# Kernel optimization log

Measured on AMD Instinct MI355X. Metric: run time of the kernel, lower is better.

The kernel has to match this reference:

```python
import jax, jax.numpy as jnp
import numpy as np

D_MODEL = 768
D_LATENT = 12288
K = 20
N = 16384


def setup_inputs() -> dict:
    key = jax.random.key(0)
    k1, k2, k3, k4, k5 = jax.random.split(key, 5)
    x = jax.random.normal(k1, (N, D_MODEL), dtype=jnp.float32)
    # nn.Linear default init scale ~ 1/sqrt(fan_in)
    W_enc = jax.random.normal(k2, (D_LATENT, D_MODEL), dtype=jnp.float32) / np.sqrt(D_MODEL)
    b_enc = jax.random.normal(k3, (D_LATENT,), dtype=jnp.float32) * 0.01
    W_dec = jax.random.normal(k4, (D_MODEL, D_LATENT), dtype=jnp.float32) / np.sqrt(D_LATENT)
    b_dec = jax.random.normal(k5, (D_MODEL,), dtype=jnp.float32) * 0.01
    return {"x": x, "W_enc": W_enc, "b_enc": b_enc, "W_dec": W_dec, "b_dec": b_dec}


def reference(x, W_enc, b_enc, W_dec, b_dec):
    # encode: [N, 12288]
    latents = jnp.einsum('nd,ld->nl', x, W_enc) + b_enc
    # top-k(20) per row; scatter kept values back into zeros == latents * mask
    vals, idx = jax.lax.top_k(latents, K)            # [N, K]
    rows = jnp.arange(latents.shape[0])[:, None]      # [N, 1]
    sparse = jnp.zeros_like(latents).at[rows, idx].set(vals)
    # decode: [N, 768]
    recons = jnp.einsum('nl,dl->nd', sparse, W_dec) + b_dec
    return recons
```

## Files before the change

### kernel.cpp

```cpp
#include <hip/hip_runtime.h>
#include <hip/hip_bf16.h>
#include <stdint.h>

#define D_MODEL_  768
#define D_LATENT_ 12288
#define N_ROWS_   16384
#define TOPK_     20
#define TOPC      16
#define NQ        8
#define NC        128
#define AUTO      12
#define NREFW     16
#define THR0      1.7f

#define BM 256
#define BN 128
#define BK 64
#define KT (D_MODEL_ / BK)
#define CTQ (D_LATENT_ / NQ / BN)
#define NTHREADS 1024
#define CAP 8

#define BUFSZ 49152

typedef float f4 __attribute__((ext_vector_type(4)));
typedef short bf16x8 __attribute__((ext_vector_type(8)));

typedef const void __attribute__((address_space(1)))* gptr_t;
typedef void __attribute__((address_space(3)))* lptr_t;

__device__ __forceinline__ void stage16(const void* g, void* l) {
  __builtin_amdgcn_global_load_lds((gptr_t)g, (lptr_t)l, 16, 0, 0);
}

__device__ __forceinline__ unsigned short bf16_rne(float f) {
  unsigned u = __builtin_bit_cast(unsigned, f);
  u += 0x7FFFu + ((u >> 16) & 1u);
  return (unsigned short)(u >> 16);
}
__device__ __forceinline__ float bf16_to_f(unsigned short h) {
  return __builtin_bit_cast(float, ((unsigned)h) << 16);
}
__device__ __forceinline__ unsigned packcand(float v, int idx) {
  return v > 0.f ? (((unsigned)bf16_rne(v) << 16) | (unsigned)idx) : 0u;
}

#define BAR_LGKM() do { asm volatile("s_waitcnt lgkmcnt(0)" ::: "memory"); \
                        __builtin_amdgcn_s_barrier(); } while (0)

__global__ void tobf16_kernel(const float4* __restrict__ in, ushort4* __restrict__ o, int n4) {
  int i = blockIdx.x * blockDim.x + threadIdx.x;
  if (i >= n4) return;
  float4 v = in[i];
  ushort4 h;
  h.x = bf16_rne(v.x); h.y = bf16_rne(v.y); h.z = bf16_rne(v.z); h.w = bf16_rne(v.w);
  o[i] = h;
}

__global__ void transpose_bf16_kernel(const float* __restrict__ wd, unsigned short* __restrict__ wdT) {
  __shared__ float tile[32][33];
  const int l0 = blockIdx.x * 32;
  const int d0 = blockIdx.y * 32;
  const int tx = threadIdx.x, ty = threadIdx.y;
#pragma unroll
  for (int i = 0; i < 32; i += 8)
    tile[ty + i][tx] = wd[(size_t)(d0 + ty + i) * D_LATENT_ + l0 + tx];
  __syncthreads();
#pragma unroll
  for (int i = 0; i < 32; i += 8)
    wdT[(size_t)(l0 + ty + i) * D_MODEL_ + d0 + tx] = bf16_rne(tile[tx][ty + i]);
}

__global__ __launch_bounds__(NTHREADS, 4) void sae_topk(
    const unsigned short* __restrict__ xh, const unsigned short* __restrict__ wh,
    const float* __restrict__ b_enc, unsigned* __restrict__ candp)
{
  __shared__ __align__(16) unsigned char smem[2 * BUFSZ];
  __shared__ unsigned s_top[BM][TOPC];
  __shared__ unsigned s_cand[BM][CAP];
  __shared__ float    s_thr[BM];
  __shared__ int      s_cnt[BM];
  __shared__ int      s_flag;

  const int tid  = threadIdx.x;
  const int lane = tid & 63;
  const int wid  = tid >> 6;
  const int wm   = wid >> 2;
  const int wn   = wid & 3;
  const int quar = blockIdx.x & 7;
  const int brow = (blockIdx.x >> 3) * BM;
  const int cbase = quar * (D_LATENT_ / NQ);

  auto stage_tile = [&](int buf, int ct, int kt) {
    unsigned char* base = smem + buf * BUFSZ;
#pragma unroll
    for (int j = 0; j < 2; ++j) {
      const int cid = tid + j * 1024;
      const int row = cid >> 3, slot = cid & 7;
      stage16(xh + (size_t)(brow + row) * D_MODEL_ + kt * BK + (slot ^ (row & 7)) * 8,
              base + cid * 16);
    }
    {
      const int row = tid >> 3, slot = tid & 7;
      stage16(wh + (size_t)(cbase + ct * BN + row) * D_MODEL_ + kt * BK + (slot ^ (row & 7)) * 8,
              base + 32768 + tid * 16);
    }
  };

  stage_tile(0, 0, 0);

  if (tid < BM) { s_thr[tid] = THR0; s_cnt[tid] = 0; }
  if (tid == 0) s_flag = 0;
  for (int i = tid; i < BM * TOPC; i += NTHREADS) (&s_top[0][0])[i] = 0u;

  f4 acc[4][2];
#pragma unroll
  for (int m = 0; m < 4; ++m)
#pragma unroll
    for (int n = 0; n < 2; ++n) { f4 z = {0.f, 0.f, 0.f, 0.f}; acc[m][n] = z; }

  int cur = 0;
#pragma unroll 1
  for (int ct = 0; ct < CTQ; ++ct) {
    const float be0 = b_enc[cbase + ct * BN + wn * 32 + (lane & 15)];
    const float be1 = b_enc[cbase + ct * BN + wn * 32 + 16 + (lane & 15)];

#pragma unroll 1
    for (int kt = 0; kt < KT; ++kt) {
      bool more = true;
      if (kt < KT - 1)       stage_tile(cur ^ 1, ct, kt + 1);
      else if (ct + 1 < CTQ) stage_tile(cur ^ 1, ct + 1, 0);
      else                   more = false;
      if (more) { asm volatile("s_waitcnt vmcnt(3)" ::: "memory"); }
      else      { asm volatile("s_waitcnt vmcnt(0)" ::: "memory"); }
      __builtin_amdgcn_s_barrier();
      {
        const unsigned char* base = smem + cur * BUFSZ;
#pragma unroll
        for (int ks = 0; ks < 2; ++ks) {
          const int c = ks * 4 + (lane >> 4);
          bf16x8 ah[4], bh[2];
#pragma unroll
          for (int m = 0; m < 4; ++m) {
            const int row = wm * 64 + m * 16 + (lane & 15);
            ah[m] = *(const bf16x8*)(base + row * 128 + ((c ^ (row & 7)) << 4));
          }
#pragma unroll
          for (int n = 0; n < 2; ++n) {
            const int col = wn * 32 + n * 16 + (lane & 15);
            bh[n] = *(const bf16x8*)(base + 32768 + col * 128 + ((c ^ (col & 7)) << 4));
          }
#pragma unroll
          for (int m = 0; m < 4; ++m)
#pragma unroll
            for (int n = 0; n < 2; ++n)
              acc[m][n] = __builtin_amdgcn_mfma_f32_16x16x32_bf16(ah[m], bh[n], acc[m][n], 0, 0, 0);
        }
      }
      __builtin_amdgcn_s_barrier();
      cur ^= 1;
    }

#pragma unroll
    for (int m = 0; m < 4; ++m) {
      acc[m][0][0] += be0; acc[m][0][1] += be0; acc[m][0][2] += be0; acc[m][0][3] += be0;
      acc[m][1][0] += be1; acc[m][1][1] += be1; acc[m][1][2] += be1; acc[m][1][3] += be1;
    }

    unsigned pend = ~0u;
#pragma unroll 1
    for (;;) {
#pragma unroll
      for (int m = 0; m < 4; ++m)
#pragma unroll
        for (int n = 0; n < 2; ++n)
#pragma unroll
          for (int j = 0; j < 4; ++j) {
            const int b = m * 8 + n * 4 + j;
            if (pend & (1u << b)) {
              const int row = wm * 64 + m * 16 + ((lane >> 4) << 2) + j;
              const float v = acc[m][n][j];
              if (v <= s_thr[row]) {
                pend &= ~(1u << b);
              } else {
                const int pos = atomicAdd(&s_cnt[row], 1);
                if (pos < CAP) {
                  s_cand[row][pos] = packcand(v, cbase + ct * BN + wn * 32 + n * 16 + (lane & 15));
                  pend &= ~(1u << b);
                }
              }
            }
          }
      BAR_LGKM();
      if (tid < BM) {
        const int row = tid;
        const int nc = s_cnt[row];
        if (nc > 0) {
          if (nc > CAP) s_flag = 1;
          unsigned minp = s_top[row][0]; int mpos = 0;
#pragma unroll
          for (int k = 1; k < TOPC; ++k) { const unsigned t = s_top[row][k]; if (t < minp) { minp = t; mpos = k; } }
          const int ne = nc < CAP ? nc : CAP;
          for (int j = 0; j < ne; ++j) {
            const unsigned p = s_cand[row][j];
            if (p > minp) {
              s_top[row][mpos] = p;
              minp = s_top[row][0]; mpos = 0;
#pragma unroll
              for (int k = 1; k < TOPC; ++k) { const unsigned t = s_top[row][k]; if (t < minp) { minp = t; mpos = k; } }
            }
          }
          const float mv = bf16_to_f((unsigned short)(minp >> 16));
          s_thr[row] = mv > THR0 ? mv : THR0;
          s_cnt[row] = 0;
        }
      }
      BAR_LGKM();
      const int f = s_flag;
      BAR_LGKM();
      if (!f) break;
      if (tid == 0) s_flag = 0;
    }

#pragma unroll
    for (int m = 0; m < 4; ++m)
#pragma unroll
      for (int n = 0; n < 2; ++n) { f4 z = {0.f, 0.f, 0.f, 0.f}; acc[m][n] = z; }
  }

  if (tid < BM) {
#pragma unroll
    for (int k = 0; k < TOPC; ++k)
      candp[(size_t)(brow + tid) * NC + quar * TOPC + k] = s_top[tid][k];
  }
}

__device__ __forceinline__ float chunk_fma(const float* __restrict__ xr,
                                           const float* __restrict__ wr,
                                           int beg, int end) {
  float a = 0.f;
#pragma unroll 4
  for (int d0 = beg; d0 < end; d0 += 4) {
    const float4 xv = *(const float4*)(xr + d0);
    const float4 wv = *(const float4*)(wr + d0);
    a = fmaf(xv.x, wv.x, a);
    a = fmaf(xv.y, wv.y, a);
    a = fmaf(xv.z, wv.z, a);
    a = fmaf(xv.w, wv.w, a);
  }
  return a;
}

__global__ __launch_bounds__(256) void refine_decode13(
    const float* __restrict__ x, const float* __restrict__ W_enc,
    const float* __restrict__ b_enc, const unsigned* __restrict__ candp,
    const unsigned short* __restrict__ wdTb, const float* __restrict__ b_dec,
    float* __restrict__ out)
{
  __shared__ unsigned s_p[4][NC];
  __shared__ unsigned s_ref[4][NREFW];
  __shared__ float s_rv[4][NREFW];
  __shared__ int   s_rid[4][NREFW];
  __shared__ float s_selv[4][TOPK_];
  __shared__ int   s_seli[4][TOPK_];

  const int tid  = threadIdx.x;
  const int w    = tid >> 6;
  const int lane = tid & 63;
  const int row  = blockIdx.x * 4 + w;

  s_p[w][lane]      = candp[(size_t)row * NC + lane];
  s_p[w][lane + 64] = candp[(size_t)row * NC + lane + 64];
  if (lane < NREFW) s_ref[w][lane] = 0u;
  __syncthreads();

#pragma unroll
  for (int t = 0; t < 2; ++t) {
    const int i = lane + t * 64;
    const unsigned p = s_p[w][i];
    if (p != 0u) {
      int r = 0;
#pragma unroll 1
      for (int j = 0; j < NC; ++j) r += (s_p[w][j] > p);
      if (r < AUTO) {
        s_selv[w][r] = bf16_to_f((unsigned short)(p >> 16));
        s_seli[w][r] = (int)(p & 0x3FFFu);
      } else if (r < AUTO + NREFW) {
        s_ref[w][r - AUTO] = p;
      }
    }
  }
  __syncthreads();

  {
    const int cand  = lane & 15;
    const int chunk = lane >> 4;
    float part = 0.f;
    const unsigned p = s_ref[w][cand];
    if (p != 0u && chunk < 3) {
      const int idx = (int)(p & 0x3FFFu);
      const float* xr = x + (size_t)row * D_MODEL_;
      const float* wr = W_enc + (size_t)idx * D_MODEL_;
      const int beg = chunk == 0 ? 0 : (chunk == 1 ? 320 : 544);
      const int end = chunk == 0 ? 320 : (chunk == 1 ? 544 : 768);
      part = chunk_fma(xr, wr, beg, end);
    }
    const float a2 = __shfl(part, cand + 16);
    const float a3 = __shfl(part, cand + 32);
    if (chunk == 0 && lane < NREFW) {
      if (p != 0u) {
        s_rv[w][lane]  = ((part + a2) + a3) + b_enc[(int)(p & 0x3FFFu)];
        s_rid[w][lane] = (int)(p & 0x3FFFu);
      } else {
        s_rv[w][lane]  = -__builtin_inff();
        s_rid[w][lane] = -1;
      }
    }
  }
  __syncthreads();

  if (lane < NREFW) {
    const float v = s_rv[w][lane]; const int id = s_rid[w][lane];
    if (id >= 0) {
      int rank = 0;
#pragma unroll 1
      for (int j = 0; j < NREFW; ++j) {
        const float vj = s_rv[w][j];
        rank += (vj > v) || (vj == v && s_rid[w][j] > id);
      }
      if (rank < TOPK_ - AUTO) { s_selv[w][AUTO + rank] = v; s_seli[w][AUTO + rank] = id; }
    }
  }
  __syncthreads();

#pragma unroll 1
  for (int r = 0; r < 4; ++r) {
#pragma unroll
    for (int j = 0; j < 3; ++j) {
      const int d = tid + j * 256;
      float a = b_dec[d];
#pragma unroll
      for (int k = 0; k < TOPK_; ++k)
        a = fmaf(s_selv[r][k], bf16_to_f(wdTb[(size_t)s_seli[r][k] * D_MODEL_ + d]), a);
      out[(size_t)(blockIdx.x * 4 + r) * D_MODEL_ + d] = a;
    }
  }
}

extern "C" void kernel_launch(void* const* d_in, const int* in_sizes, int n_in,
                              void* d_out, int out_size, void* d_ws, size_t ws_size,
                              hipStream_t stream) {
  const float* x     = (const float*)d_in[0];
  const float* W_enc = (const float*)d_in[1];
  const float* b_enc = (const float*)d_in[2];
  const float* W_dec = (const float*)d_in[3];
  const float* b_dec = (const float*)d_in[4];
  float* out = (float*)d_out;
  char* ws = (char*)d_ws;

  unsigned short* xh = (unsigned short*)(ws + 0);
  unsigned short* wh = (unsigned short*)(ws + 25165824);
  unsigned*     candp = (unsigned*)(ws + 44040192);
  unsigned short* wdTb = (unsigned short*)(ws + 0);

  {
    int n4 = N_ROWS_ * D_MODEL_ / 4;
    tobf16_kernel<<<(n4 + 255) / 256, 256, 0, stream>>>((const float4*)x, (ushort4*)xh, n4);
  }
  {
    int n4 = D_LATENT_ * D_MODEL_ / 4;
    tobf16_kernel<<<(n4 + 255) / 256, 256, 0, stream>>>((const float4*)W_enc, (ushort4*)wh, n4);
  }

  sae_topk<<<(N_ROWS_ / BM) * NQ, NTHREADS, 0, stream>>>(xh, wh, b_enc, candp);

  transpose_bf16_kernel<<<dim3(D_LATENT_ / 32, D_MODEL_ / 32), dim3(32, 8), 0, stream>>>(W_dec, wdTb);

  refine_decode13<<<N_ROWS_ / 4, 256, 0, stream>>>(x, W_enc, b_enc, candp, wdTb, b_dec, out);
}
```

Measured before the change: 823.2 us.

## Stage GEMM tiles through registers and cut a barrier from top-k rounds

Replaces the direct global-to-LDS async loads with register-staged loads: the next tile is loaded into registers before the MFMA work and written to the other LDS buffer afterwards. This drops one barrier per k-step. The top-k overflow flag becomes a per-round array so the retry loop needs one fewer barrier per round, with the flags reset after each column tile. The trade-off is extra VGPR pressure under 1024-thread launch bounds, and the vmcnt(0) wait before the write can expose load latency that the old async path hid.

```diff
diff --git a/kernel.cpp b/kernel.cpp
--- a/kernel.cpp
+++ b/kernel.cpp
@@ -12,6 +12,7 @@
 #define AUTO      12
 #define NREFW     16
 #define THR0      1.7f
+#define MAXR      8
 
 #define BM 256
 #define BN 128
@@ -25,13 +26,6 @@
 
 typedef float f4 __attribute__((ext_vector_type(4)));
 typedef short bf16x8 __attribute__((ext_vector_type(8)));
-
-typedef const void __attribute__((address_space(1)))* gptr_t;
-typedef void __attribute__((address_space(3)))* lptr_t;
-
-__device__ __forceinline__ void stage16(const void* g, void* l) {
-  __builtin_amdgcn_global_load_lds((gptr_t)g, (lptr_t)l, 16, 0, 0);
-}
 
 __device__ __forceinline__ unsigned short bf16_rne(float f) {
   unsigned u = __builtin_bit_cast(unsigned, f);
@@ -80,7 +74,7 @@
   __shared__ unsigned s_cand[BM][CAP];
   __shared__ float    s_thr[BM];
   __shared__ int      s_cnt[BM];
-  __shared__ int      s_flag;
+  __shared__ int      s_flag[MAXR];
 
   const int tid  = threadIdx.x;
   const int lane = tid & 63;
@@ -91,26 +85,36 @@
   const int brow = (blockIdx.x >> 3) * BM;
   const int cbase = quar * (D_LATENT_ / NQ);
 
-  auto stage_tile = [&](int buf, int ct, int kt) {
+  const int a_row0 = tid >> 3,           a_slot0 = tid & 7;
+  const int a_row1 = (tid + 1024) >> 3,  a_slot1 = tid & 7;
+  const unsigned short* a_src0 = xh + (size_t)(brow + a_row0) * D_MODEL_ + (a_slot0 ^ (a_row0 & 7)) * 8;
+  const unsigned short* a_src1 = xh + (size_t)(brow + a_row1) * D_MODEL_ + (a_slot1 ^ (a_row1 & 7)) * 8;
+  const int b_row = tid >> 3,            b_slot = tid & 7;
+  const unsigned short* b_src = wh + (size_t)(cbase + b_row) * D_MODEL_ + (b_slot ^ (b_row & 7)) * 8;
+
+  const int a_dst0 = tid * 16;
+  const int a_dst1 = (tid + 1024) * 16;
+  const int b_dst  = 32768 + tid * 16;
+
+  float4 ra0, ra1, rb;
+
+  auto stage_load = [&](int ct, int kt) {
+    const int ko = kt * BK;
+    ra0 = *(const float4*)(a_src0 + ko);
+    ra1 = *(const float4*)(a_src1 + ko);
+    rb  = *(const float4*)(b_src + (size_t)ct * BN * D_MODEL_ + ko);
+  };
+  auto stage_write = [&](int buf) {
     unsigned char* base = smem + buf * BUFSZ;
-#pragma unroll
-    for (int j = 0; j < 2; ++j) {
-      const int cid = tid + j * 1024;
-      const int row = cid >> 3, slot = cid & 7;
-      stage16(xh + (size_t)(brow + row) * D_MODEL_ + kt * BK + (slot ^ (row & 7)) * 8,
-              base + cid * 16);
-    }
-    {
-      const int row = tid >> 3, slot = tid & 7;
-      stage16(wh + (size_t)(cbase + ct * BN + row) * D_MODEL_ + kt * BK + (slot ^ (row & 7)) * 8,
-              base + 32768 + tid * 16);
-    }
+    *(float4*)(base + a_dst0) = ra0;
+    *(float4*)(base + a_dst1) = ra1;
+    *(float4*)(base + b_dst)  = rb;
   };
 
-  stage_tile(0, 0, 0);
+  stage_load(0, 0);
 
   if (tid < BM) { s_thr[tid] = THR0; s_cnt[tid] = 0; }
-  if (tid == 0) s_flag = 0;
+  if (tid < MAXR) s_flag[tid] = 0;
   for (int i = tid; i < BM * TOPC; i += NTHREADS) (&s_top[0][0])[i] = 0u;
 
   f4 acc[4][2];
@@ -118,6 +122,10 @@
   for (int m = 0; m < 4; ++m)
 #pragma unroll
     for (int n = 0; n < 2; ++n) { f4 z = {0.f, 0.f, 0.f, 0.f}; acc[m][n] = z; }
+
+  asm volatile("s_waitcnt vmcnt(0)" ::: "memory");
+  stage_write(0);
+  BAR_LGKM();
 
   int cur = 0;
 #pragma unroll 1
@@ -128,12 +136,9 @@
 #pragma unroll 1
     for (int kt = 0; kt < KT; ++kt) {
       bool more = true;
-      if (kt < KT - 1)       stage_tile(cur ^ 1, ct, kt + 1);
-      else if (ct + 1 < CTQ) stage_tile(cur ^ 1, ct + 1, 0);
+      if (kt < KT - 1)       stage_load(ct, kt + 1);
+      else if (ct + 1 < CTQ) stage_load(ct + 1, 0);
       else                   more = false;
-      if (more) { asm volatile("s_waitcnt vmcnt(3)" ::: "memory"); }
-      else      { asm volatile("s_waitcnt vmcnt(0)" ::: "memory"); }
-      __builtin_amdgcn_s_barrier();
       {
         const unsigned char* base = smem + cur * BUFSZ;
 #pragma unroll
@@ -157,7 +162,11 @@
               acc[m][n] = __builtin_amdgcn_mfma_f32_16x16x32_bf16(ah[m], bh[n], acc[m][n], 0, 0, 0);
         }
       }
-      __builtin_amdgcn_s_barrier();
+      if (more) {
+        asm volatile("s_waitcnt vmcnt(0)" ::: "memory");
+        stage_write(cur ^ 1);
+      }
+      BAR_LGKM();
       cur ^= 1;
     }
 
@@ -169,7 +178,7 @@
 
     unsigned pend = ~0u;
 #pragma unroll 1
-    for (;;) {
+    for (int rnd = 0; ; ++rnd) {
 #pragma unroll
       for (int m = 0; m < 4; ++m)
 #pragma unroll
@@ -196,7 +205,7 @@
         const int row = tid;
         const int nc = s_cnt[row];
         if (nc > 0) {
-          if (nc > CAP) s_flag = 1;
+          if (nc > CAP) s_flag[(rnd + 1) < MAXR ? (rnd + 1) : (MAXR - 1)] = 1;
           unsigned minp = s_top[row][0]; int mpos = 0;
 #pragma unroll
           for (int k = 1; k < TOPC; ++k) { const unsigned t = s_top[row][k]; if (t < minp) { minp = t; mpos = k; } }
@@ -216,11 +225,12 @@
         }
       }
       BAR_LGKM();
-      const int f = s_flag;
+      const int nxt = (rnd + 1) < MAXR ? (rnd + 1) : (MAXR - 1);
+      if (!s_flag[nxt]) break;
+      if (tid == 0) s_flag[nxt] = 0;
       BAR_LGKM();
-      if (!f) break;
-      if (tid == 0) s_flag = 0;
-    }
+    }
+    if (tid < MAXR) s_flag[tid] = 0;
 
 #pragma unroll
     for (int m = 0; m < 4; ++m)
```

New measurement: 861.8 us. 1.05x slower.
